# Kernel optimization log

Measured on AMD Instinct MI355X. Metric: run time of the kernel, lower is better.

## Reference

```python
import jax, jax.numpy as jnp
import numpy as np

WINDOW_SIZE = 11
SIGMA = 1.5
DATA_RANGE = 1.0
C1 = (0.01 * DATA_RANGE) ** 2
C2 = (0.03 * DATA_RANGE) ** 2


def _gaussian_window(size: int, sigma: float) -> jnp.ndarray:
    coords = jnp.arange(size, dtype=jnp.float32) - size // 2
    g = jnp.exp(-(coords ** 2) / (2.0 * sigma ** 2))
    g = g / g.sum()
    w2d = g[:, None] * g[None, :]
    return w2d[None, None, :, :]  # (O=1, I=1, K, K)


def _conv_same(x, window):
    pad = WINDOW_SIZE // 2
    return jax.lax.conv_general_dilated(
        x, window,
        window_strides=(1, 1),
        padding=((pad, pad), (pad, pad)),
        dimension_numbers=("NCHW", "OIHW", "NCHW"),
    )


def setup_inputs() -> dict:
    key = jax.random.key(0)
    kx, ky = jax.random.split(key)
    B, C, H, W = 64, 1, 512, 512
    x = jax.random.uniform(kx, (B, C, H, W), dtype=jnp.float32)
    y = jax.random.uniform(ky, (B, C, H, W), dtype=jnp.float32)
    return {"x": x, "y": y}


def reference(x, y):
    window = _gaussian_window(WINDOW_SIZE, SIGMA)
    mu_x = _conv_same(x, window)
    mu_y = _conv_same(y, window)
    mu_x_sq = mu_x * mu_x
    mu_y_sq = mu_y * mu_y
    mu_xy = mu_x * mu_y
    sigma_x_sq = _conv_same(x * x, window) - mu_x_sq
    sigma_y_sq = _conv_same(y * y, window) - mu_y_sq
    sigma_xy = _conv_same(x * y, window) - mu_xy
    num = (2.0 * mu_xy + C1) * (2.0 * sigma_xy + C2)
    den = (mu_x_sq + mu_y_sq + C1) * (sigma_x_sq + sigma_y_sq + C2)
    ssim_map = num / den
    ssim_val = ssim_map.mean(axis=(1, 2, 3))  # (B,)
    loss = 1.0 - ssim_val
    return loss.mean()  # reduction='mean'
```

## Files before the change

### kernel.cpp

```cpp
#include <hip/hip_runtime.h>
#include <hip/hip_fp16.h>

typedef _Float16 f16x8 __attribute__((ext_vector_type(8)));
typedef float    f32x4 __attribute__((ext_vector_type(4)));
typedef float    f32x2 __attribute__((ext_vector_type(2)));

#define IMG   512
#define NIMG  64
#define TS_C  64
#define NBLK  (NIMG * 8 * 8)
#define XST   88
#define HTS   36
#define SROWS 42

#define C1F   1.0e-4f
#define C2F   9.0e-4f
#define INVSUM 0.26601174f

__device__ __forceinline__ uint2 cvt4h(f32x4 a) {
    __half2 p0 = __floats2half2_rn(a[0], a[1]);
    __half2 p1 = __floats2half2_rn(a[2], a[3]);
    uint2 r; r.x = *reinterpret_cast<uint*>(&p0); r.y = *reinterpret_cast<uint*>(&p1);
    return r;
}

__global__ __launch_bounds__(256, 4)
void ssim_main(const float* __restrict__ x, const float* __restrict__ y,
               float* __restrict__ partial) {
    __shared__ __align__(16) __half XYp[2 * SROWS * XST];
    __shared__ __align__(16) __half Ht[3][TS_C][HTS];
    __shared__ float red[4];

    const int tid  = threadIdx.x;
    const int lane = tid & 63;
    const int wv   = tid >> 6;
    const int l16  = lane & 15;
    const int g16  = lane >> 4;
    const int n0   = wv * 16;

    const int img = blockIdx.z;
    const int by  = blockIdx.y;
    const int c0  = blockIdx.x * TS_C;
    const float* xb = x + (size_t)img * IMG * IMG;
    const float* yb = y + (size_t)img * IMG * IMG;

    const int row0 = tid / 20;
    const int c40  = tid - row0 * 20;

    auto stage_load = [&](int r0, float4* st) {
        bool interior = (r0 >= 8) & (r0 <= IMG - 37) & (c0 >= 8) & (c0 <= IMG - 72);
        int row_u = row0, c4 = c40;
        #pragma unroll
        for (int i = 0; i < 7; ++i) {
            int  ru = row_u > 83 ? 83 : row_u;
            bool ya = ru >= SROWS;
            int  rp = ya ? ru - SROWS : ru;
            int  gr = r0 - 5 + rp;
            int  gc = c0 - 8 + c4 * 4;
            const float* src = (ya ? yb : xb) + (size_t)gr * IMG + gc;
            if (interior) {
                st[i] = *(const float4*)src;
            } else {
                bool valid = (i < 6) | (tid < 144);
                bool ok = valid & ((unsigned)gr < (unsigned)IMG) & ((unsigned)gc < (unsigned)IMG);
                st[i] = ok ? *(const float4*)src : make_float4(0.f, 0.f, 0.f, 0.f);
            }
            c4 += 16; int inc = 12;
            if (c4 >= 20) { c4 -= 20; inc = 13; }
            row_u += inc;
        }
    };

    auto stage_write = [&](const float4* st) {
        int row_u = row0, c4 = c40;
        #pragma unroll
        for (int i = 0; i < 7; ++i) {
            if (i < 6 || tid < 144) {
                __half2 p0 = __floats2half2_rn(st[i].x, st[i].y);
                __half2 p1 = __floats2half2_rn(st[i].z, st[i].w);
                uint2 v; v.x = *reinterpret_cast<uint*>(&p0); v.y = *reinterpret_cast<uint*>(&p1);
                *(uint2*)&XYp[row_u * XST + c4 * 4] = v;
            }
            c4 += 16; int inc = 12;
            if (c4 >= 20) { c4 -= 20; inc = 13; }
            row_u += inc;
        }
    };

    const int hcol = n0 + l16;
    f32x2 ssum2 = {0.0f, 0.0f};
    f16x8 WhB, WvA;

    auto hpassA = [&](int g, int sb) {
        int srow = g * 16 + l16;
        if (srow > SROWS - 1) srow = SROWS - 1;
        int off = srow * XST + n0 + g16 * 8;
        f16x8 xf = *(const f16x8*)&XYp[off];
        f16x8 yf = *(const f16x8*)&XYp[SROWS * XST + off];
        f16x8 xy = xf * yf;
        f32x4 z = {0.f, 0.f, 0.f, 0.f};
        f32x4 aX  = __builtin_amdgcn_mfma_f32_16x16x32_f16(xf, WhB, z, 0, 0, 0);
        f32x4 aY  = __builtin_amdgcn_mfma_f32_16x16x32_f16(yf, WhB, z, 0, 0, 0);
        f32x4 aXY = __builtin_amdgcn_mfma_f32_16x16x32_f16(xy, WhB, z, 0, 0, 0);
        int hrow = sb + g16 * 4;
        *(uint2*)&Ht[0][hcol][hrow] = cvt4h(aX);
        *(uint2*)&Ht[1][hcol][hrow] = cvt4h(aY);
        *(uint2*)&Ht[2][hcol][hrow] = cvt4h(aXY);
    };

    auto hpassB = [&](int g, int sb) {
        int srow = g * 16 + l16;
        if (srow > SROWS - 1) srow = SROWS - 1;
        int off = srow * XST + n0 + g16 * 8;
        f16x8 xf = *(const f16x8*)&XYp[off];
        f16x8 yf = *(const f16x8*)&XYp[SROWS * XST + off];
        f16x8 xx = xf * xf;
        f16x8 yy = yf * yf;
        f32x4 z = {0.f, 0.f, 0.f, 0.f};
        f32x4 aXX = __builtin_amdgcn_mfma_f32_16x16x32_f16(xx, WhB, z, 0, 0, 0);
        f32x4 aYY = __builtin_amdgcn_mfma_f32_16x16x32_f16(yy, WhB, z, 0, 0, 0);
        int hrow = sb + g16 * 4;
        *(uint2*)&Ht[0][hcol][hrow] = cvt4h(aXX);
        *(uint2*)&Ht[1][hcol][hrow] = cvt4h(aYY);
    };

    auto vpassA = [&](int mt, f32x4& oX, f32x4& oY, f32x4& oXY) {
        int ko = (mt * 16 + g16 * 8) & 31;
        f16x8 b0 = *(const f16x8*)&Ht[0][hcol][ko];
        f16x8 b1 = *(const f16x8*)&Ht[1][hcol][ko];
        f16x8 b2 = *(const f16x8*)&Ht[2][hcol][ko];
        f32x4 z = {0.f, 0.f, 0.f, 0.f};
        oX  = __builtin_amdgcn_mfma_f32_16x16x32_f16(WvA, b0, z, 0, 0, 0);
        oY  = __builtin_amdgcn_mfma_f32_16x16x32_f16(WvA, b1, z, 0, 0, 0);
        oXY = __builtin_amdgcn_mfma_f32_16x16x32_f16(WvA, b2, z, 0, 0, 0);
    };

    auto vpassB = [&](int mt, f32x4 vXm, f32x4 vYm, f32x4 vXYm) {
        int ko = (mt * 16 + g16 * 8) & 31;
        f16x8 b0 = *(const f16x8*)&Ht[0][hcol][ko];
        f16x8 b1 = *(const f16x8*)&Ht[1][hcol][ko];
        f32x4 z = {0.f, 0.f, 0.f, 0.f};
        f32x4 cXX = __builtin_amdgcn_mfma_f32_16x16x32_f16(WvA, b0, z, 0, 0, 0);
        f32x4 cYY = __builtin_amdgcn_mfma_f32_16x16x32_f16(WvA, b1, z, 0, 0, 0);
        #pragma unroll
        for (int h = 0; h < 2; ++h) {
            f32x2 mx  = {vXm [2*h], vXm [2*h+1]};
            f32x2 my  = {vYm [2*h], vYm [2*h+1]};
            f32x2 exx = {cXX [2*h], cXX [2*h+1]};
            f32x2 eyy = {cYY [2*h], cYY [2*h+1]};
            f32x2 exy = {vXYm[2*h], vXYm[2*h+1]};
            f32x2 mxx = mx * mx, myy = my * my, mxy = mx * my;
            f32x2 vx  = exx - mxx;
            f32x2 vy  = eyy - myy;
            f32x2 vxy = exy - mxy;
            f32x2 num = (2.0f * mxy + C1F) * (2.0f * vxy + C2F);
            f32x2 den = (mxx + myy + C1F) * (vx + vy + C2F);
            f32x2 r;
            r[0] = __builtin_amdgcn_rcpf(den[0]);
            r[1] = __builtin_amdgcn_rcpf(den[1]);
            ssum2 += num * r;
        }
    };

    auto do_tile = [&](bool wr_next, const float4* stn) {
        f32x4 cX0, cY0, cXY0, cX1, cY1, cXY1;
        hpassA(0, 0); hpassA(1, 16);
        vpassA(0, cX0, cY0, cXY0);
        hpassA(2, 0);
        vpassA(1, cX1, cY1, cXY1);
        hpassB(0, 0); hpassB(1, 16);
        vpassB(0, cX0, cY0, cXY0);
        hpassB(2, 0);
        if (wr_next) {
            __syncthreads();
            stage_write(stn);
        }
        vpassB(1, cX1, cY1, cXY1);
    };

    const int r0a = by * 64;
    const int r0b = by * 64 + 32;
    float4 st0[7], st1[7];

    stage_load(r0a, st0);
    stage_load(r0b, st1);

    {
        const int d0 = g16 * 8 - l16 - 3;
        _Float16 bv[11];
        #pragma unroll
        for (int j = 0; j < 11; ++j) {
            int d = d0 + j;
            float t = (float)(d - 5);
            float v = __expf(-t * t * (1.0f / 4.5f)) * INVSUM;
            bv[j] = ((unsigned)d <= 10u) ? (_Float16)v : (_Float16)0.0f;
        }
        #pragma unroll
        for (int j = 0; j < 8; ++j) WhB[j] = bv[j];
        #pragma unroll
        for (int j = 0; j < 8; ++j) WvA[j] = bv[j + 3];
    }

    stage_write(st0);
    __syncthreads();

    do_tile(true, st1);
    __syncthreads();
    do_tile(false, nullptr);

    float ssum = ssum2[0] + ssum2[1];
    #pragma unroll
    for (int off = 32; off > 0; off >>= 1)
        ssum += __shfl_down(ssum, off, 64);
    if ((tid & 63) == 0) red[tid >> 6] = ssum;
    __syncthreads();
    if (tid == 0) {
        float tot = red[0] + red[1] + red[2] + red[3];
        int bi = (img * gridDim.y + by) * gridDim.x + blockIdx.x;
        partial[bi] = tot;
    }
}

__global__ __launch_bounds__(1024)
void ssim_final(const float* __restrict__ partial, float* __restrict__ out) {
    __shared__ float red[16];
    float s = 0.0f;
    for (int i = threadIdx.x; i < NBLK; i += 1024) s += partial[i];
    #pragma unroll
    for (int off = 32; off > 0; off >>= 1)
        s += __shfl_down(s, off, 64);
    if ((threadIdx.x & 63) == 0) red[threadIdx.x >> 6] = s;
    __syncthreads();
    if (threadIdx.x == 0) {
        float tot = 0.0f;
        #pragma unroll
        for (int i = 0; i < 16; ++i) tot += red[i];
        out[0] = 1.0f - tot * (1.0f / 16777216.0f);
    }
}

extern "C" void kernel_launch(void* const* d_in, const int* in_sizes, int n_in,
                              void* d_out, int out_size, void* d_ws, size_t ws_size,
                              hipStream_t stream) {
    const float* x = (const float*)d_in[0];
    const float* y = (const float*)d_in[1];
    float* out     = (float*)d_out;
    float* partial = (float*)d_ws;

    dim3 grid(IMG / TS_C, 8, NIMG);
    ssim_main<<<grid, 256, 0, stream>>>(x, y, partial);
    ssim_final<<<1, 1024, 0, stream>>>(partial, out);
}
```

Before: 46.88 us.

## Give each wave a private haloed staging window and drop block-wide barriers

Each wave now loads its own 32-column slice of x and y, with the 8-column halo on each side, into a private LDS region. Because no wave reads another wave's staged data, the two __syncthreads around staging are removed and waves run independently. The second tile's global load is issued midway through the first tile's compute rather than up front, which overlaps latency and lowers peak register use. In exchange, halo columns are loaded redundantly by neighbouring waves, LDS use per block roughly doubles, and launch bounds drop from 4 to 3 blocks per CU.

```diff
diff --git a/kernel.cpp b/kernel.cpp
--- a/kernel.cpp
+++ b/kernel.cpp
@@ -9,9 +9,10 @@
 #define NIMG  64
 #define TS_C  64
 #define NBLK  (NIMG * 8 * 8)
-#define XST   88
+#define XWS   36
+#define PL    (42 * XWS)
+#define WVS   (2 * PL)
 #define HTS   36
-#define SROWS 42
 
 #define C1F   1.0e-4f
 #define C2F   9.0e-4f
@@ -24,10 +25,10 @@
     return r;
 }
 
-__global__ __launch_bounds__(256, 4)
+__global__ __launch_bounds__(256, 3)
 void ssim_main(const float* __restrict__ x, const float* __restrict__ y,
                float* __restrict__ partial) {
-    __shared__ __align__(16) __half XYp[2 * SROWS * XST];
+    __shared__ __align__(16) __half XW[4 * WVS];
     __shared__ __align__(16) __half Ht[3][TS_C][HTS];
     __shared__ float red[4];
 
@@ -44,46 +45,41 @@
     const float* xb = x + (size_t)img * IMG * IMG;
     const float* yb = y + (size_t)img * IMG * IMG;
 
-    const int row0 = tid / 20;
-    const int c40  = tid - row0 * 20;
-
-    auto stage_load = [&](int r0, float4* st) {
-        bool interior = (r0 >= 8) & (r0 <= IMG - 37) & (c0 >= 8) & (c0 <= IMG - 72);
-        int row_u = row0, c4 = c40;
-        #pragma unroll
-        for (int i = 0; i < 7; ++i) {
-            int  ru = row_u > 83 ? 83 : row_u;
-            bool ya = ru >= SROWS;
-            int  rp = ya ? ru - SROWS : ru;
-            int  gr = r0 - 5 + rp;
-            int  gc = c0 - 8 + c4 * 4;
-            const float* src = (ya ? yb : xb) + (size_t)gr * IMG + gc;
-            if (interior) {
-                st[i] = *(const float4*)src;
-            } else {
-                bool valid = (i < 6) | (tid < 144);
-                bool ok = valid & ((unsigned)gr < (unsigned)IMG) & ((unsigned)gc < (unsigned)IMG);
-                st[i] = ok ? *(const float4*)src : make_float4(0.f, 0.f, 0.f, 0.f);
-            }
-            c4 += 16; int inc = 12;
-            if (c4 >= 20) { c4 -= 20; inc = 13; }
-            row_u += inc;
+    const int xwb = wv * WVS;
+
+    auto stage_issue = [&](int r0t, float4* st) {
+        #pragma unroll
+        for (int i = 0; i < 11; ++i) {
+            int  u     = i * 64 + lane;
+            bool valid = u < 672;
+            int  e     = valid ? u : 0;
+            bool pl    = e >= 336;
+            int  e2    = pl ? e - 336 : e;
+            int  row   = e2 >> 3;
+            int  u4    = e2 & 7;
+            int  gr    = r0t - 5 + row;
+            int  gc    = c0 + n0 - 8 + u4 * 4;
+            bool ok    = valid & ((unsigned)gr < (unsigned)IMG)
+                               & ((unsigned)gc <= (unsigned)(IMG - 4));
+            const float* src = (pl ? yb : xb) + (size_t)gr * IMG + gc;
+            st[i] = ok ? *(const float4*)src : make_float4(0.f, 0.f, 0.f, 0.f);
         }
     };
 
     auto stage_write = [&](const float4* st) {
-        int row_u = row0, c4 = c40;
-        #pragma unroll
-        for (int i = 0; i < 7; ++i) {
-            if (i < 6 || tid < 144) {
+        #pragma unroll
+        for (int i = 0; i < 11; ++i) {
+            int u = i * 64 + lane;
+            if (u < 672) {
+                bool pl = u >= 336;
+                int  e2 = pl ? u - 336 : u;
+                int  row = e2 >> 3;
+                int  u4  = e2 & 7;
                 __half2 p0 = __floats2half2_rn(st[i].x, st[i].y);
                 __half2 p1 = __floats2half2_rn(st[i].z, st[i].w);
                 uint2 v; v.x = *reinterpret_cast<uint*>(&p0); v.y = *reinterpret_cast<uint*>(&p1);
-                *(uint2*)&XYp[row_u * XST + c4 * 4] = v;
+                *(uint2*)&XW[xwb + (pl ? PL : 0) + row * XWS + u4 * 4] = v;
             }
-            c4 += 16; int inc = 12;
-            if (c4 >= 20) { c4 -= 20; inc = 13; }
-            row_u += inc;
         }
     };
 
@@ -93,10 +89,10 @@
 
     auto hpassA = [&](int g, int sb) {
         int srow = g * 16 + l16;
-        if (srow > SROWS - 1) srow = SROWS - 1;
-        int off = srow * XST + n0 + g16 * 8;
-        f16x8 xf = *(const f16x8*)&XYp[off];
-        f16x8 yf = *(const f16x8*)&XYp[SROWS * XST + off];
+        if (srow > 41) srow = 41;
+        int off = xwb + srow * XWS + g16 * 8;
+        f16x8 xf = *(const f16x8*)&XW[off];
+        f16x8 yf = *(const f16x8*)&XW[off + PL];
         f16x8 xy = xf * yf;
         f32x4 z = {0.f, 0.f, 0.f, 0.f};
         f32x4 aX  = __builtin_amdgcn_mfma_f32_16x16x32_f16(xf, WhB, z, 0, 0, 0);
@@ -110,10 +106,10 @@
 
     auto hpassB = [&](int g, int sb) {
         int srow = g * 16 + l16;
-        if (srow > SROWS - 1) srow = SROWS - 1;
-        int off = srow * XST + n0 + g16 * 8;
-        f16x8 xf = *(const f16x8*)&XYp[off];
-        f16x8 yf = *(const f16x8*)&XYp[SROWS * XST + off];
+        if (srow > 41) srow = 41;
+        int off = xwb + srow * XWS + g16 * 8;
+        f16x8 xf = *(const f16x8*)&XW[off];
+        f16x8 yf = *(const f16x8*)&XW[off + PL];
         f16x8 xx = xf * xf;
         f16x8 yy = yf * yf;
         f32x4 z = {0.f, 0.f, 0.f, 0.f};
@@ -162,7 +158,44 @@
         }
     };
 
-    auto do_tile = [&](bool wr_next, const float4* stn) {
+    const int r0a = by * 64;
+    const int r0b = by * 64 + 32;
+    float4 st0[11], st1[11];
+
+    stage_issue(r0a, st0);
+
+    {
+        const int d0 = g16 * 8 - l16 - 3;
+        _Float16 bv[11];
+        #pragma unroll
+        for (int j = 0; j < 11; ++j) {
+            int d = d0 + j;
+            float t = (float)(d - 5);
+            float v = __expf(-t * t * (1.0f / 4.5f)) * INVSUM;
+            bv[j] = ((unsigned)d <= 10u) ? (_Float16)v : (_Float16)0.0f;
+        }
+        #pragma unroll
+        for (int j = 0; j < 8; ++j) WhB[j] = bv[j];
+        #pragma unroll
+        for (int j = 0; j < 8; ++j) WvA[j] = bv[j + 3];
+    }
+
+    stage_write(st0);
+
+    {
+        f32x4 cX0, cY0, cXY0, cX1, cY1, cXY1;
+        hpassA(0, 0); hpassA(1, 16);
+        vpassA(0, cX0, cY0, cXY0);
+        hpassA(2, 0);
+        vpassA(1, cX1, cY1, cXY1);
+        stage_issue(r0b, st1);
+        hpassB(0, 0); hpassB(1, 16);
+        vpassB(0, cX0, cY0, cXY0);
+        hpassB(2, 0);
+        vpassB(1, cX1, cY1, cXY1);
+    }
+    stage_write(st1);
+    {
         f32x4 cX0, cY0, cXY0, cX1, cY1, cXY1;
         hpassA(0, 0); hpassA(1, 16);
         vpassA(0, cX0, cY0, cXY0);
@@ -171,42 +204,8 @@
         hpassB(0, 0); hpassB(1, 16);
         vpassB(0, cX0, cY0, cXY0);
         hpassB(2, 0);
-        if (wr_next) {
-            __syncthreads();
-            stage_write(stn);
-        }
         vpassB(1, cX1, cY1, cXY1);
-    };
-
-    const int r0a = by * 64;
-    const int r0b = by * 64 + 32;
-    float4 st0[7], st1[7];
-
-    stage_load(r0a, st0);
-    stage_load(r0b, st1);
-
-    {
-        const int d0 = g16 * 8 - l16 - 3;
-        _Float16 bv[11];
-        #pragma unroll
-        for (int j = 0; j < 11; ++j) {
-            int d = d0 + j;
-            float t = (float)(d - 5);
-            float v = __expf(-t * t * (1.0f / 4.5f)) * INVSUM;
-            bv[j] = ((unsigned)d <= 10u) ? (_Float16)v : (_Float16)0.0f;
-        }
-        #pragma unroll
-        for (int j = 0; j < 8; ++j) WhB[j] = bv[j];
-        #pragma unroll
-        for (int j = 0; j < 8; ++j) WvA[j] = bv[j + 3];
-    }
-
-    stage_write(st0);
-    __syncthreads();
-
-    do_tile(true, st1);
-    __syncthreads();
-    do_tile(false, nullptr);
+    }
 
     float ssum = ssum2[0] + ssum2[1];
     #pragma unroll
```

After: 59.83 us. 1.28x slower.

## Shrink blocks to 32x32 tiles with 128 threads and drop staged double tile

Applied to the files above, without the earlier changes.

Reworks the tiling so each block handles one 32x32 output tile with two wavefronts instead of a 64-column by 64-row region processed as two software-pipelined row tiles. The grid grows to 16x16 tiles per image, and the prefetch/stage-write overlap between tiles is removed in favour of one load-convert-compute pass. The intent is more blocks and better latency hiding through parallelism. The cost is a larger halo overhead: 42x48 staged input per 32x32 output, which means more redundant global loads and horizontal-pass work per output pixel.

```diff
diff --git a/kernel.cpp b/kernel.cpp
--- a/kernel.cpp
+++ b/kernel.cpp
@@ -7,11 +7,11 @@
 
 #define IMG   512
 #define NIMG  64
-#define TS_C  64
-#define NBLK  (NIMG * 8 * 8)
-#define XST   88
+#define NBLK  (NIMG * 16 * 16)
+#define XST2  52
+#define PL2   (42 * XST2)
+#define UNITS 1008
 #define HTS   36
-#define SROWS 42
 
 #define C1F   1.0e-4f
 #define C2F   9.0e-4f
@@ -24,12 +24,12 @@
     return r;
 }
 
-__global__ __launch_bounds__(256, 4)
+__global__ __launch_bounds__(128, 3)
 void ssim_main(const float* __restrict__ x, const float* __restrict__ y,
                float* __restrict__ partial) {
-    __shared__ __align__(16) __half XYp[2 * SROWS * XST];
-    __shared__ __align__(16) __half Ht[3][TS_C][HTS];
-    __shared__ float red[4];
+    __shared__ __align__(16) __half XYp[2 * PL2];
+    __shared__ __align__(16) __half Ht[3][32][HTS];
+    __shared__ float red[2];
 
     const int tid  = threadIdx.x;
     const int lane = tid & 63;
@@ -40,63 +40,80 @@
 
     const int img = blockIdx.z;
     const int by  = blockIdx.y;
-    const int c0  = blockIdx.x * TS_C;
+    const int r0  = by * 32;
+    const int c0  = blockIdx.x * 32;
     const float* xb = x + (size_t)img * IMG * IMG;
     const float* yb = y + (size_t)img * IMG * IMG;
 
-    const int row0 = tid / 20;
-    const int c40  = tid - row0 * 20;
-
-    auto stage_load = [&](int r0, float4* st) {
-        bool interior = (r0 >= 8) & (r0 <= IMG - 37) & (c0 >= 8) & (c0 <= IMG - 72);
+    const int row0 = tid / 12;
+    const int c40  = tid - row0 * 12;
+    float4 st[8];
+    {
         int row_u = row0, c4 = c40;
         #pragma unroll
-        for (int i = 0; i < 7; ++i) {
+        for (int i = 0; i < 8; ++i) {
+            bool valid = (i < 7) | (tid < UNITS - 7 * 128);
             int  ru = row_u > 83 ? 83 : row_u;
-            bool ya = ru >= SROWS;
-            int  rp = ya ? ru - SROWS : ru;
+            bool pl = ru >= 42;
+            int  rp = pl ? ru - 42 : ru;
             int  gr = r0 - 5 + rp;
             int  gc = c0 - 8 + c4 * 4;
-            const float* src = (ya ? yb : xb) + (size_t)gr * IMG + gc;
-            if (interior) {
-                st[i] = *(const float4*)src;
-            } else {
-                bool valid = (i < 6) | (tid < 144);
-                bool ok = valid & ((unsigned)gr < (unsigned)IMG) & ((unsigned)gc < (unsigned)IMG);
-                st[i] = ok ? *(const float4*)src : make_float4(0.f, 0.f, 0.f, 0.f);
-            }
-            c4 += 16; int inc = 12;
-            if (c4 >= 20) { c4 -= 20; inc = 13; }
+            bool ok = valid & ((unsigned)gr < (unsigned)IMG)
+                            & ((unsigned)gc <= (unsigned)(IMG - 4));
+            const float* src = (pl ? yb : xb) + (size_t)gr * IMG + gc;
+            st[i] = ok ? *(const float4*)src : make_float4(0.f, 0.f, 0.f, 0.f);
+            c4 += 8; int inc = 10;
+            if (c4 >= 12) { c4 -= 12; inc = 11; }
             row_u += inc;
         }
-    };
-
-    auto stage_write = [&](const float4* st) {
+    }
+
+    f16x8 WhB, WvA;
+    {
+        const int d0 = g16 * 8 - l16 - 3;
+        _Float16 bv[11];
+        #pragma unroll
+        for (int j = 0; j < 11; ++j) {
+            int d = d0 + j;
+            float t = (float)(d - 5);
+            float v = __expf(-t * t * (1.0f / 4.5f)) * INVSUM;
+            bv[j] = ((unsigned)d <= 10u) ? (_Float16)v : (_Float16)0.0f;
+        }
+        #pragma unroll
+        for (int j = 0; j < 8; ++j) WhB[j] = bv[j];
+        #pragma unroll
+        for (int j = 0; j < 8; ++j) WvA[j] = bv[j + 3];
+    }
+
+    {
         int row_u = row0, c4 = c40;
         #pragma unroll
-        for (int i = 0; i < 7; ++i) {
-            if (i < 6 || tid < 144) {
+        for (int i = 0; i < 8; ++i) {
+            if (i < 7 || tid < UNITS - 7 * 128) {
+                int  ru = row_u;
+                bool pl = ru >= 42;
+                int  rp = pl ? ru - 42 : ru;
                 __half2 p0 = __floats2half2_rn(st[i].x, st[i].y);
                 __half2 p1 = __floats2half2_rn(st[i].z, st[i].w);
                 uint2 v; v.x = *reinterpret_cast<uint*>(&p0); v.y = *reinterpret_cast<uint*>(&p1);
-                *(uint2*)&XYp[row_u * XST + c4 * 4] = v;
+                *(uint2*)&XYp[(pl ? PL2 : 0) + rp * XST2 + c4 * 4] = v;
             }
-            c4 += 16; int inc = 12;
-            if (c4 >= 20) { c4 -= 20; inc = 13; }
+            c4 += 8; int inc = 10;
+            if (c4 >= 12) { c4 -= 12; inc = 11; }
             row_u += inc;
         }
-    };
+    }
+    __syncthreads();
 
     const int hcol = n0 + l16;
     f32x2 ssum2 = {0.0f, 0.0f};
-    f16x8 WhB, WvA;
 
     auto hpassA = [&](int g, int sb) {
         int srow = g * 16 + l16;
-        if (srow > SROWS - 1) srow = SROWS - 1;
-        int off = srow * XST + n0 + g16 * 8;
+        if (srow > 41) srow = 41;
+        int off = srow * XST2 + n0 + g16 * 8;
         f16x8 xf = *(const f16x8*)&XYp[off];
-        f16x8 yf = *(const f16x8*)&XYp[SROWS * XST + off];
+        f16x8 yf = *(const f16x8*)&XYp[PL2 + off];
         f16x8 xy = xf * yf;
         f32x4 z = {0.f, 0.f, 0.f, 0.f};
         f32x4 aX  = __builtin_amdgcn_mfma_f32_16x16x32_f16(xf, WhB, z, 0, 0, 0);
@@ -110,10 +127,10 @@
 
     auto hpassB = [&](int g, int sb) {
         int srow = g * 16 + l16;
-        if (srow > SROWS - 1) srow = SROWS - 1;
-        int off = srow * XST + n0 + g16 * 8;
+        if (srow > 41) srow = 41;
+        int off = srow * XST2 + n0 + g16 * 8;
         f16x8 xf = *(const f16x8*)&XYp[off];
-        f16x8 yf = *(const f16x8*)&XYp[SROWS * XST + off];
+        f16x8 yf = *(const f16x8*)&XYp[PL2 + off];
         f16x8 xx = xf * xf;
         f16x8 yy = yf * yf;
         f32x4 z = {0.f, 0.f, 0.f, 0.f};
@@ -162,7 +179,7 @@
         }
     };
 
-    auto do_tile = [&](bool wr_next, const float4* stn) {
+    {
         f32x4 cX0, cY0, cXY0, cX1, cY1, cXY1;
         hpassA(0, 0); hpassA(1, 16);
         vpassA(0, cX0, cY0, cXY0);
@@ -171,42 +188,8 @@
         hpassB(0, 0); hpassB(1, 16);
         vpassB(0, cX0, cY0, cXY0);
         hpassB(2, 0);
-        if (wr_next) {
-            __syncthreads();
-            stage_write(stn);
-        }
         vpassB(1, cX1, cY1, cXY1);
-    };
-
-    const int r0a = by * 64;
-    const int r0b = by * 64 + 32;
-    float4 st0[7], st1[7];
-
-    stage_load(r0a, st0);
-    stage_load(r0b, st1);
-
-    {
-        const int d0 = g16 * 8 - l16 - 3;
-        _Float16 bv[11];
-        #pragma unroll
-        for (int j = 0; j < 11; ++j) {
-            int d = d0 + j;
-            float t = (float)(d - 5);
-            float v = __expf(-t * t * (1.0f / 4.5f)) * INVSUM;
-            bv[j] = ((unsigned)d <= 10u) ? (_Float16)v : (_Float16)0.0f;
-        }
-        #pragma unroll
-        for (int j = 0; j < 8; ++j) WhB[j] = bv[j];
-        #pragma unroll
-        for (int j = 0; j < 8; ++j) WvA[j] = bv[j + 3];
-    }
-
-    stage_write(st0);
-    __syncthreads();
-
-    do_tile(true, st1);
-    __syncthreads();
-    do_tile(false, nullptr);
+    }
 
     float ssum = ssum2[0] + ssum2[1];
     #pragma unroll
@@ -215,9 +198,8 @@
     if ((tid & 63) == 0) red[tid >> 6] = ssum;
     __syncthreads();
     if (tid == 0) {
-        float tot = red[0] + red[1] + red[2] + red[3];
         int bi = (img * gridDim.y + by) * gridDim.x + blockIdx.x;
-        partial[bi] = tot;
+        partial[bi] = red[0] + red[1];
     }
 }
 
@@ -247,7 +229,7 @@
     float* out     = (float*)d_out;
     float* partial = (float*)d_ws;
 
-    dim3 grid(IMG / TS_C, 8, NIMG);
-    ssim_main<<<grid, 256, 0, stream>>>(x, y, partial);
+    dim3 grid(IMG / 32, IMG / 32, NIMG);
+    ssim_main<<<grid, 128, 0, stream>>>(x, y, partial);
     ssim_final<<<1, 1024, 0, stream>>>(partial, out);
 }
```

Measured after the change: 70.89 us. 51.2% more time.

## Stage full 74-row halo tile once instead of two overlapping 42-row subtiles

Applied to the files above, without the earlier changes.

Loads the whole 64+10 row strip for x and y into shared memory in a single staging pass rather than two 42-row subtiles that each reload a 10-row halo. The second sub-tile now reads from an offset into the same buffer, which removes the duplicated halo loads and the mid-kernel barrier plus rewrite. In exchange, shared memory per block nearly doubles, launch bounds drop to 3 blocks per CU, and each thread holds 12 float4 staging registers, which lowers occupancy and loses the overlap of the second tile's load with the first tile's compute.

```diff
diff --git a/kernel.cpp b/kernel.cpp
--- a/kernel.cpp
+++ b/kernel.cpp
@@ -11,7 +11,9 @@
 #define NBLK  (NIMG * 8 * 8)
 #define XST   88
 #define HTS   36
-#define SROWS 42
+#define SR2   74
+#define PLN   (SR2 * XST)
+#define UNITS (2 * SR2 * 20)
 
 #define C1F   1.0e-4f
 #define C2F   9.0e-4f
@@ -24,10 +26,10 @@
     return r;
 }
 
-__global__ __launch_bounds__(256, 4)
+__global__ __launch_bounds__(256, 3)
 void ssim_main(const float* __restrict__ x, const float* __restrict__ y,
                float* __restrict__ partial) {
-    __shared__ __align__(16) __half XYp[2 * SROWS * XST];
+    __shared__ __align__(16) __half XYp[2 * PLN];
     __shared__ __align__(16) __half Ht[3][TS_C][HTS];
     __shared__ float red[4];
 
@@ -44,24 +46,26 @@
     const float* xb = x + (size_t)img * IMG * IMG;
     const float* yb = y + (size_t)img * IMG * IMG;
 
+    const int rbase = by * 64;
+
     const int row0 = tid / 20;
     const int c40  = tid - row0 * 20;
 
-    auto stage_load = [&](int r0, float4* st) {
-        bool interior = (r0 >= 8) & (r0 <= IMG - 37) & (c0 >= 8) & (c0 <= IMG - 72);
+    auto stage_load = [&](float4* st) {
+        bool interior = (blockIdx.x >= 1) & (blockIdx.x <= 6) & (by >= 1) & (by <= 6);
         int row_u = row0, c4 = c40;
         #pragma unroll
-        for (int i = 0; i < 7; ++i) {
-            int  ru = row_u > 83 ? 83 : row_u;
-            bool ya = ru >= SROWS;
-            int  rp = ya ? ru - SROWS : ru;
-            int  gr = r0 - 5 + rp;
+        for (int i = 0; i < 12; ++i) {
+            int  ru = row_u > 147 ? 147 : row_u;
+            bool ya = ru >= SR2;
+            int  rp = ya ? ru - SR2 : ru;
+            int  gr = rbase - 5 + rp;
             int  gc = c0 - 8 + c4 * 4;
             const float* src = (ya ? yb : xb) + (size_t)gr * IMG + gc;
             if (interior) {
                 st[i] = *(const float4*)src;
             } else {
-                bool valid = (i < 6) | (tid < 144);
+                bool valid = (i < 11) | (tid < UNITS - 11 * 256);
                 bool ok = valid & ((unsigned)gr < (unsigned)IMG) & ((unsigned)gc < (unsigned)IMG);
                 st[i] = ok ? *(const float4*)src : make_float4(0.f, 0.f, 0.f, 0.f);
             }
@@ -74,8 +78,8 @@
     auto stage_write = [&](const float4* st) {
         int row_u = row0, c4 = c40;
         #pragma unroll
-        for (int i = 0; i < 7; ++i) {
-            if (i < 6 || tid < 144) {
+        for (int i = 0; i < 12; ++i) {
+            if (i < 11 || tid < UNITS - 11 * 256) {
                 __half2 p0 = __floats2half2_rn(st[i].x, st[i].y);
                 __half2 p1 = __floats2half2_rn(st[i].z, st[i].w);
                 uint2 v; v.x = *reinterpret_cast<uint*>(&p0); v.y = *reinterpret_cast<uint*>(&p1);
@@ -91,12 +95,12 @@
     f32x2 ssum2 = {0.0f, 0.0f};
     f16x8 WhB, WvA;
 
-    auto hpassA = [&](int g, int sb) {
-        int srow = g * 16 + l16;
-        if (srow > SROWS - 1) srow = SROWS - 1;
+    auto hpassA = [&](int base, int g, int sb) {
+        int srow = base + g * 16 + l16;
+        if (srow > SR2 - 1) srow = SR2 - 1;
         int off = srow * XST + n0 + g16 * 8;
         f16x8 xf = *(const f16x8*)&XYp[off];
-        f16x8 yf = *(const f16x8*)&XYp[SROWS * XST + off];
+        f16x8 yf = *(const f16x8*)&XYp[PLN + off];
         f16x8 xy = xf * yf;
         f32x4 z = {0.f, 0.f, 0.f, 0.f};
         f32x4 aX  = __builtin_amdgcn_mfma_f32_16x16x32_f16(xf, WhB, z, 0, 0, 0);
@@ -108,12 +112,12 @@
         *(uint2*)&Ht[2][hcol][hrow] = cvt4h(aXY);
     };
 
-    auto hpassB = [&](int g, int sb) {
-        int srow = g * 16 + l16;
-        if (srow > SROWS - 1) srow = SROWS - 1;
+    auto hpassB = [&](int base, int g, int sb) {
+        int srow = base + g * 16 + l16;
+        if (srow > SR2 - 1) srow = SR2 - 1;
         int off = srow * XST + n0 + g16 * 8;
         f16x8 xf = *(const f16x8*)&XYp[off];
-        f16x8 yf = *(const f16x8*)&XYp[SROWS * XST + off];
+        f16x8 yf = *(const f16x8*)&XYp[PLN + off];
         f16x8 xx = xf * xf;
         f16x8 yy = yf * yf;
         f32x4 z = {0.f, 0.f, 0.f, 0.f};
@@ -162,28 +166,20 @@
         }
     };
 
-    auto do_tile = [&](bool wr_next, const float4* stn) {
+    auto do_tile = [&](int base) {
         f32x4 cX0, cY0, cXY0, cX1, cY1, cXY1;
-        hpassA(0, 0); hpassA(1, 16);
+        hpassA(base, 0, 0); hpassA(base, 1, 16);
         vpassA(0, cX0, cY0, cXY0);
-        hpassA(2, 0);
+        hpassA(base, 2, 0);
         vpassA(1, cX1, cY1, cXY1);
-        hpassB(0, 0); hpassB(1, 16);
+        hpassB(base, 0, 0); hpassB(base, 1, 16);
         vpassB(0, cX0, cY0, cXY0);
-        hpassB(2, 0);
-        if (wr_next) {
-            __syncthreads();
-            stage_write(stn);
-        }
+        hpassB(base, 2, 0);
         vpassB(1, cX1, cY1, cXY1);
     };
 
-    const int r0a = by * 64;
-    const int r0b = by * 64 + 32;
-    float4 st0[7], st1[7];
-
-    stage_load(r0a, st0);
-    stage_load(r0b, st1);
+    float4 st[12];
+    stage_load(st);
 
     {
         const int d0 = g16 * 8 - l16 - 3;
@@ -201,12 +197,11 @@
         for (int j = 0; j < 8; ++j) WvA[j] = bv[j + 3];
     }
 
-    stage_write(st0);
+    stage_write(st);
     __syncthreads();
 
-    do_tile(true, st1);
-    __syncthreads();
-    do_tile(false, nullptr);
+    do_tile(0);
+    do_tile(32);
 
     float ssum = ssum2[0] + ssum2[1];
     #pragma unroll
```

Result: no change. 46.67 us (-0.5%).
